# Performance work log

Measured on AMD Instinct MI355X. Metric: run time of the kernel, lower is better.

Reference implementation:

```python
import jax, jax.numpy as jnp
import numpy as np

HEADS = 8

def setup_inputs() -> dict:
    key = jax.random.key(0)
    ks = jax.random.split(key, 10)
    B, C, D, W, H = 4, 256, 12, 12, 12
    dk = C // HEADS
    return {
        "x": jax.random.normal(ks[0], (B, C, D, W, H), jnp.float32),
        "wq": jax.random.normal(ks[1], (C, C), jnp.float32) * 0.05,
        "bq": jax.random.normal(ks[2], (C,), jnp.float32) * 0.05,
        "wk": jax.random.normal(ks[3], (C, C), jnp.float32) * 0.05,
        "bk": jax.random.normal(ks[4], (C,), jnp.float32) * 0.05,
        "wv": jax.random.normal(ks[5], (C, C), jnp.float32) * 0.05,
        "bv": jax.random.normal(ks[6], (C,), jnp.float32) * 0.05,
        "rel_d": jax.random.normal(ks[7], (1, HEADS, dk, D, 1, 1), jnp.float32),
        "rel_h": jax.random.normal(ks[8], (1, HEADS, dk, 1, 1, H), jnp.float32),
        "rel_w": jax.random.normal(ks[9], (1, HEADS, dk, 1, W, 1), jnp.float32),
    }


def reference(x, wq, bq, wk, bk, wv, bv, rel_d, rel_h, rel_w):
    B, C, D, W, H = x.shape
    dk = C // HEADS
    N = D * W * H

    def proj(w, b):
        # Conv3d kernel_size=1 == per-voxel linear over channels
        y = jnp.einsum('bcdwh,oc->bodwh', x, w) + b[None, :, None, None, None]
        return y.reshape(B, HEADS, dk, N)  # [B,h,dk,N]

    q = proj(wq, bq)
    k = proj(wk, bk)
    v = proj(wv, bv)

    # content-content: q^T k -> [B,h,N,N]
    cc = jnp.einsum('bhdn,bhdm->bhnm', q, k)
    # relative-position bias: (rel_h+rel_w+rel_d) broadcasts to [1,h,dk,D,W,H]
    pos = (rel_h + rel_w + rel_d).reshape(1, HEADS, dk, N)
    # content-position: pos^T @ q -> [B,h,N,N]
    cp = jnp.einsum('bhdn,bhdm->bhnm', pos, q)

    attn = jax.nn.softmax(cc + cp, axis=-1)  # [B,h,N,N]
    # out = v @ attn^T -> [B,h,dk,N]
    out = jnp.einsum('bhdn,bhmn->bhdm', v, attn)
    return out.reshape(B, C, D, W, H)
```

## Files before the change

kernel.cpp:

```cpp
#include <hip/hip_runtime.h>
#include <math.h>

#define HEADS 8
#define DK 32
#define B_ 4
#define C_ 256
#define NVOX 1728
#define DE 64
#define PITCH 72
#define XPITCH 136
#define CPITCH 36
#define LOG2E 1.44269504088896f

typedef _Float16 f16x8 __attribute__((ext_vector_type(8)));
typedef float f32x16 __attribute__((ext_vector_type(16)));

__device__ inline float h2f(short s) {
    _Float16 h = *(_Float16*)&s;
    return (float)h;
}
__device__ inline f32x16 mfma32h(f16x8 a, f16x8 b, f32x16 c) {
    return __builtin_amdgcn_mfma_f32_32x32x16_f16(a, b, c, 0, 0, 0);
}

union H8 { _Float16 h[8]; uint4 v; };
union H4 { _Float16 h[4]; uint2 v; };

__global__ void wf16_kernel(const float* __restrict__ wq,
                            const float* __restrict__ wk,
                            const float* __restrict__ wv,
                            short* __restrict__ wf) {
    int idx = blockIdx.x * 256 + threadIdx.x;
    int m = idx >> 16;
    const float* w = (m == 0) ? wq : (m == 1) ? wk : wv;
    _Float16 h = (_Float16)w[idx & 65535];
    wf[idx] = *(short*)&h;
}

__global__ __launch_bounds__(256)
void xf16_kernel(const float* __restrict__ x, short* __restrict__ xf) {
    __shared__ float tile[64][65];
    int nb = blockIdx.x * 64, c0 = blockIdx.y * 64, b = blockIdx.z;
    int t = threadIdx.x;
    const float* xb = x + (size_t)b * C_ * NVOX;
    for (int e = t; e < 4096; e += 256) {
        int ci = e >> 6, nl = e & 63;
        tile[ci][nl] = xb[(size_t)(c0 + ci) * NVOX + nb + nl];
    }
    __syncthreads();
    for (int e = t; e < 512; e += 256) {
        int n = e >> 3, cg = (e & 7) * 8;
        H8 hi;
        #pragma unroll
        for (int j = 0; j < 8; j++) hi.h[j] = (_Float16)tile[cg + j][n];
        size_t off = ((size_t)b * NVOX + nb + n) * C_ + c0 + cg;
        *(uint4*)&xf[off] = hi.v;
    }
}

__global__ void pos_kernel(const float* __restrict__ rel_d,
                           const float* __restrict__ rel_h,
                           const float* __restrict__ rel_w,
                           short* __restrict__ Qf) {
    int t = threadIdx.x;
    int nl = t & 63, dd0 = (t >> 6) * 8;
    int n = blockIdx.x * 64 + nl;
    int h = blockIdx.y, b = blockIdx.z;
    int bh = b * HEADS + h;
    int di = n / 144, wi = (n / 12) % 12, hi = n % 12;
    H8 ph;
    #pragma unroll
    for (int o = 0; o < 8; o++) {
        int hd = h * DK + dd0 + o;
        ph.h[o] = (_Float16)(rel_d[hd * 12 + di] + rel_w[hd * 12 + wi] + rel_h[hd * 12 + hi]);
    }
    *(uint4*)&Qf[((size_t)bh * NVOX + n) * DE + DK + dd0] = ph.v;
}

struct FS {
    union {
        short xs[64 * XPITCH];
        float cbuf[3][64][CPITCH];
    } u;
};

__global__ __launch_bounds__(384, 4)
void fproj_kernel(const short* __restrict__ xf, const short* __restrict__ wf,
                  const float* __restrict__ bq, const float* __restrict__ bk,
                  const float* __restrict__ bv,
                  short* __restrict__ Qf, short* __restrict__ Kf,
                  short* __restrict__ Vf) {
    __shared__ FS sm;
    int nb = blockIdx.x * 64, h = blockIdx.y, b = blockIdx.z;
    int bh = b * HEADS + h;
    int t = threadIdx.x;
    int w = t >> 6, l = t & 63, ln = l & 31, hv = l >> 5;
    int mat = w >> 1, nh = w & 1;

    const short* xb = xf + ((size_t)b * NVOX + nb) * C_;
    const short* wA = wf + ((size_t)mat * C_ + h * DK + ln) * C_;
    int xrow = (nh * 32 + ln) * XPITCH;

    f32x16 acc;
    #pragma unroll
    for (int r = 0; r < 16; r++) acc[r] = 0.f;

    #pragma unroll 1
    for (int ch = 0; ch < 2; ch++) {
        __syncthreads();
        for (int e = t; e < 1024; e += 384) {
            int row = e >> 4, c8 = (e & 15) * 8;
            *(uint4*)&sm.u.xs[row * XPITCH + c8] =
                *(const uint4*)&xb[row * C_ + ch * 128 + c8];
        }
        __syncthreads();
        #pragma unroll 4
        for (int ks = 0; ks < 8; ks++) {
            int kl_ = ks * 16 + hv * 8;
            f16x8 a = *(const f16x8*)&wA[ch * 128 + kl_];
            f16x8 bfr = *(const f16x8*)&sm.u.xs[xrow + kl_];
            acc = mfma32h(a, bfr, acc);
        }
    }
    __syncthreads();

    const float* bias = (mat == 0) ? bq : (mat == 1) ? bk : bv;
    int ncol = nh * 32 + ln;
    #pragma unroll
    for (int q2 = 0; q2 < 4; q2++) {
        float4 cv;
        float* cvp = (float*)&cv;
        #pragma unroll
        for (int m = 0; m < 4; m++) {
            int o_loc = 8 * q2 + 4 * hv + m;
            cvp[m] = acc[4 * q2 + m] + bias[h * DK + o_loc];
        }
        *(float4*)&sm.u.cbuf[mat][ncol][8 * q2 + 4 * hv] = cv;
    }
    __syncthreads();

    if (t < 256) {
        int n = t >> 2, ddg = (t & 3) * 8;
        size_t rowoff = ((size_t)bh * NVOX + nb + n) * DE;
        H8 qh, kh;
        #pragma unroll
        for (int j = 0; j < 8; j++) {
            qh.h[j] = (_Float16)sm.u.cbuf[0][n][ddg + j];
            kh.h[j] = (_Float16)sm.u.cbuf[1][n][ddg + j];
        }
        *(uint4*)&Qf[rowoff + ddg] = qh.v;
        *(uint4*)&Kf[rowoff + ddg] = kh.v;
        *(uint4*)&Kf[rowoff + DK + ddg] = qh.v;
    }
    if (t < 256) {
        int d = t >> 3, ng = (t & 7) * 8;
        H8 vv;
        #pragma unroll
        for (int j = 0; j < 8; j++)
            vv.h[j] = (_Float16)sm.u.cbuf[2][ng + j][d];
        *(uint4*)&Vf[((size_t)bh * DK + d) * NVOX + nb + ng] = vv.v;
    }
}

struct SMem {
    short K[64][PITCH];
    short V[DK][PITCH];
    short P[96][PITCH];
};

__global__ __launch_bounds__(192, 4)
void attn_kernel(const short* __restrict__ Qf, const short* __restrict__ Kf,
                 const short* __restrict__ Vf,
                 short* __restrict__ wsO, float* __restrict__ wsM,
                 float* __restrict__ wsL) {
    __shared__ SMem sm;
    int bx = blockIdx.x;
    int it = bx / 3, jp = bx % 3;
    int h = blockIdx.y, b = blockIdx.z;
    int bh = b * HEADS + h;
    int t = threadIdx.x;
    int w  = t >> 6;
    int l  = t & 63;
    int ln = l & 31;
    int hv = l >> 5;
    int i_loc  = w * 32 + ln;
    int i_glob = it * 96 + i_loc;

    const short* Qp = Qf + (size_t)bh * NVOX * DE;
    const short* Kp = Kf + (size_t)bh * NVOX * DE;
    const short* Vp = Vf + (size_t)bh * DK * NVOX;

    f16x8 qf[4];
    #pragma unroll
    for (int ks = 0; ks < 4; ks++)
        qf[ks] = *(const f16x8*)&Qp[(size_t)i_glob * DE + ks * 16 + hv * 8];

    float mL = -INFINITY;
    float lsum = 0.f;
    f32x16 O;
    #pragma unroll
    for (int r = 0; r < 16; r++) O[r] = 0.f;

    int jt0 = jp * 9, jt1 = jt0 + 9;
    #pragma unroll 1
    for (int jt = jt0; jt < jt1; jt++) {
        int jb = jt * 64;
        __syncthreads();
        for (int e = t; e < 512; e += 192) {
            int row = e >> 3, c = (e & 7) * 8;
            *(uint4*)&sm.K[row][c] = *(const uint4*)&Kp[(size_t)(jb + row) * DE + c];
        }
        for (int e = t; e < 256; e += 192) {
            int d = e >> 3, c = (e & 7) * 8;
            *(uint4*)&sm.V[d][c] = *(const uint4*)&Vp[(size_t)d * NVOX + jb + c];
        }
        __syncthreads();

        f32x16 sc[2];
        #pragma unroll
        for (int js = 0; js < 2; js++) {
            f32x16 s;
            #pragma unroll
            for (int r = 0; r < 16; r++) s[r] = 0.f;
            #pragma unroll
            for (int ks = 0; ks < 4; ks++) {
                f16x8 kfr = *(const f16x8*)&sm.K[js * 32 + ln][ks * 16 + hv * 8];
                s = mfma32h(kfr, qf[ks], s);
            }
            sc[js] = s;
        }

        float mx = sc[0][0];
        #pragma unroll
        for (int js = 0; js < 2; js++)
            #pragma unroll
            for (int r = 0; r < 16; r++) mx = fmaxf(mx, sc[js][r]);
        mx = fmaxf(mx, __shfl_xor(mx, 32));
        float mLn = fmaxf(mL, mx * LOG2E);
        float alpha = exp2f(mL - mLn);
        mL = mLn;
        float ps = 0.f;
        #pragma unroll
        for (int js = 0; js < 2; js++)
            #pragma unroll
            for (int r = 0; r < 16; r++) {
                float p = exp2f(fmaf(sc[js][r], LOG2E, -mLn));
                sc[js][r] = p;
                ps += p;
            }
        ps += __shfl_xor(ps, 32);
        lsum = lsum * alpha + ps;

        #pragma unroll
        for (int js = 0; js < 2; js++)
            #pragma unroll
            for (int g = 0; g < 4; g++) {
                H4 pk;
                #pragma unroll
                for (int m = 0; m < 4; m++) pk.h[m] = (_Float16)sc[js][4 * g + m];
                *(uint2*)&sm.P[i_loc][js * 32 + g * 8 + hv * 4] = pk.v;
            }

        #pragma unroll
        for (int r = 0; r < 16; r++) O[r] *= alpha;
        #pragma unroll
        for (int ks = 0; ks < 4; ks++) {
            f16x8 va = *(const f16x8*)&sm.V[ln][ks * 16 + hv * 8];
            f16x8 pb = *(const f16x8*)&sm.P[i_loc][ks * 16 + hv * 8];
            O = mfma32h(va, pb, O);
        }
    }

    short* Op = wsO + ((size_t)jp * (B_ * HEADS) + bh) * DK * NVOX;
    #pragma unroll
    for (int r = 0; r < 16; r++) {
        int d = (r & 3) + 8 * (r >> 2) + 4 * hv;
        _Float16 oh = (_Float16)O[r];
        Op[(size_t)d * NVOX + i_glob] = *(short*)&oh;
    }
    if (hv == 0) {
        size_t mo = ((size_t)jp * (B_ * HEADS) + bh) * NVOX + i_glob;
        wsM[mo] = mL;
        wsL[mo] = lsum;
    }
}

__global__ void combine_kernel(const short* __restrict__ wsO,
                               const float* __restrict__ wsM,
                               const float* __restrict__ wsL,
                               float* __restrict__ out) {
    int idx = blockIdx.x * 256 + threadIdx.x;
    int i = idx % NVOX;
    int bh = (idx / NVOX) >> 5;
    const size_t oh = (size_t)B_ * HEADS * DK * NVOX;
    const size_t mh = (size_t)B_ * HEADS * NVOX;
    size_t mo = (size_t)bh * NVOX + i;
    float m0 = wsM[mo], m1 = wsM[mh + mo], m2 = wsM[2 * mh + mo];
    float m = fmaxf(fmaxf(m0, m1), m2);
    float a0 = exp2f(m0 - m), a1 = exp2f(m1 - m), a2 = exp2f(m2 - m);
    float num = a0 * h2f(wsO[idx]) + a1 * h2f(wsO[oh + idx]) + a2 * h2f(wsO[2 * oh + idx]);
    float den = a0 * wsL[mo] + a1 * wsL[mh + mo] + a2 * wsL[2 * mh + mo];
    out[idx] = num / den;
}

extern "C" void kernel_launch(void* const* d_in, const int* in_sizes, int n_in,
                              void* d_out, int out_size, void* d_ws, size_t ws_size,
                              hipStream_t stream) {
    const float* x     = (const float*)d_in[0];
    const float* wq    = (const float*)d_in[1];
    const float* bq    = (const float*)d_in[2];
    const float* wk    = (const float*)d_in[3];
    const float* bk    = (const float*)d_in[4];
    const float* wv    = (const float*)d_in[5];
    const float* bv    = (const float*)d_in[6];
    const float* rel_d = (const float*)d_in[7];
    const float* rel_h = (const float*)d_in[8];
    const float* rel_w = (const float*)d_in[9];
    float* out = (float*)d_out;

    size_t qksz = (size_t)B_ * HEADS * NVOX * DE;
    size_t vsz  = (size_t)B_ * HEADS * DK * NVOX;
    short* Qf  = (short*)d_ws;
    short* Kf  = Qf + qksz;
    short* Vf  = Kf + qksz;
    short* wf  = Vf + vsz;
    short* wsO = wf + (size_t)3 * C_ * C_;
    float* wsM = (float*)(wsO + 3 * vsz);
    float* wsL = wsM + 3 * (size_t)B_ * HEADS * NVOX;
    short* xf  = wsO;

    wf16_kernel<<<dim3(3 * C_ * C_ / 256), dim3(256), 0, stream>>>(wq, wk, wv, wf);
    xf16_kernel<<<dim3(NVOX / 64, C_ / 64, B_), dim3(256), 0, stream>>>(x, xf);
    pos_kernel<<<dim3(NVOX / 64, HEADS, B_), dim3(256), 0, stream>>>(
        rel_d, rel_h, rel_w, Qf);
    fproj_kernel<<<dim3(NVOX / 64, HEADS, B_), dim3(384), 0, stream>>>(
        xf, wf, bq, bk, bv, Qf, Kf, Vf);
    attn_kernel<<<dim3(3 * NVOX / 96, HEADS, B_), dim3(192), 0, stream>>>(
        Qf, Kf, Vf, wsO, wsM, wsL);
    combine_kernel<<<dim3((int)(vsz / 256)), dim3(256), 0, stream>>>(wsO, wsM, wsL, out);
}
```

Before: 165.0 us.

## Merge prep kernels, retile attention to 64-row blocks with 2-way KV split

Folds the weight cast, x transpose-cast and positional bias kernels into one prep launch dispatched by block index, removing two launches. Attention blocks shrink from 96 to 64 query rows (2 waves) and the key range is split in two parts of 14 and 13 tiles instead of three parts of 9, so the combine step merges two partials. P packing uses the packed round-toward-zero fp16 convert instead of per-element casts. Together these change grid shape, occupancy and the amount of partial output written and combined.

```diff
diff --git a/kernel.cpp b/kernel.cpp
--- a/kernel.cpp
+++ b/kernel.cpp
@@ -13,6 +13,7 @@
 #define LOG2E 1.44269504088896f
 
 typedef _Float16 f16x8 __attribute__((ext_vector_type(8)));
+typedef __fp16 fp16x2 __attribute__((ext_vector_type(2)));
 typedef float f32x16 __attribute__((ext_vector_type(16)));
 
 __device__ inline float h2f(short s) {
@@ -24,57 +25,61 @@
 }
 
 union H8 { _Float16 h[8]; uint4 v; };
-union H4 { _Float16 h[4]; uint2 v; };
-
-__global__ void wf16_kernel(const float* __restrict__ wq,
-                            const float* __restrict__ wk,
-                            const float* __restrict__ wv,
-                            short* __restrict__ wf) {
-    int idx = blockIdx.x * 256 + threadIdx.x;
-    int m = idx >> 16;
-    const float* w = (m == 0) ? wq : (m == 1) ? wk : wv;
-    _Float16 h = (_Float16)w[idx & 65535];
-    wf[idx] = *(short*)&h;
-}
 
 __global__ __launch_bounds__(256)
-void xf16_kernel(const float* __restrict__ x, short* __restrict__ xf) {
+void prep_kernel(const float* __restrict__ x,
+                 const float* __restrict__ wq, const float* __restrict__ wk,
+                 const float* __restrict__ wv,
+                 const float* __restrict__ rel_d, const float* __restrict__ rel_h,
+                 const float* __restrict__ rel_w,
+                 short* __restrict__ wf, short* __restrict__ xf,
+                 short* __restrict__ Qf) {
     __shared__ float tile[64][65];
-    int nb = blockIdx.x * 64, c0 = blockIdx.y * 64, b = blockIdx.z;
+    int bid = blockIdx.x;
     int t = threadIdx.x;
-    const float* xb = x + (size_t)b * C_ * NVOX;
-    for (int e = t; e < 4096; e += 256) {
-        int ci = e >> 6, nl = e & 63;
-        tile[ci][nl] = xb[(size_t)(c0 + ci) * NVOX + nb + nl];
-    }
-    __syncthreads();
-    for (int e = t; e < 512; e += 256) {
-        int n = e >> 3, cg = (e & 7) * 8;
-        H8 hi;
-        #pragma unroll
-        for (int j = 0; j < 8; j++) hi.h[j] = (_Float16)tile[cg + j][n];
-        size_t off = ((size_t)b * NVOX + nb + n) * C_ + c0 + cg;
-        *(uint4*)&xf[off] = hi.v;
-    }
-}
-
-__global__ void pos_kernel(const float* __restrict__ rel_d,
-                           const float* __restrict__ rel_h,
-                           const float* __restrict__ rel_w,
-                           short* __restrict__ Qf) {
-    int t = threadIdx.x;
-    int nl = t & 63, dd0 = (t >> 6) * 8;
-    int n = blockIdx.x * 64 + nl;
-    int h = blockIdx.y, b = blockIdx.z;
-    int bh = b * HEADS + h;
-    int di = n / 144, wi = (n / 12) % 12, hi = n % 12;
-    H8 ph;
-    #pragma unroll
-    for (int o = 0; o < 8; o++) {
-        int hd = h * DK + dd0 + o;
-        ph.h[o] = (_Float16)(rel_d[hd * 12 + di] + rel_w[hd * 12 + wi] + rel_h[hd * 12 + hi]);
-    }
-    *(uint4*)&Qf[((size_t)bh * NVOX + n) * DE + DK + dd0] = ph.v;
+
+    if (bid < 768) {
+        int idx = bid * 256 + t;
+        int m = idx >> 16;
+        const float* w = (m == 0) ? wq : (m == 1) ? wk : wv;
+        _Float16 h = (_Float16)w[idx & 65535];
+        wf[idx] = *(short*)&h;
+    } else if (bid < 1200) {
+        int q = bid - 768;
+        int nb = (q % 27) * 64;
+        int c0 = ((q / 27) % 4) * 64;
+        int b  = q / 108;
+        const float* xb = x + (size_t)b * C_ * NVOX;
+        for (int e = t; e < 4096; e += 256) {
+            int ci = e >> 6, nl = e & 63;
+            tile[ci][nl] = xb[(size_t)(c0 + ci) * NVOX + nb + nl];
+        }
+        __syncthreads();
+        for (int e = t; e < 512; e += 256) {
+            int n = e >> 3, cg = (e & 7) * 8;
+            H8 hi;
+            #pragma unroll
+            for (int j = 0; j < 8; j++) hi.h[j] = (_Float16)tile[cg + j][n];
+            *(uint4*)&xf[((size_t)b * NVOX + nb + n) * C_ + c0 + cg] = hi.v;
+        }
+    } else {
+        int q = bid - 1200;
+        int nb = (q % 27) * 64;
+        int h  = (q / 27) % 8;
+        int b  = q / 216;
+        int bh = b * HEADS + h;
+        int nl = t & 63, dd0 = (t >> 6) * 8;
+        int n = nb + nl;
+        int di = n / 144, wi = (n / 12) % 12, hi = n % 12;
+        H8 ph;
+        #pragma unroll
+        for (int o = 0; o < 8; o++) {
+            int hd = h * DK + dd0 + o;
+            ph.h[o] = (_Float16)(rel_d[hd * 12 + di] + rel_w[hd * 12 + wi] +
+                                 rel_h[hd * 12 + hi]);
+        }
+        *(uint4*)&Qf[((size_t)bh * NVOX + n) * DE + DK + dd0] = ph.v;
+    }
 }
 
 struct FS {
@@ -165,17 +170,17 @@
 struct SMem {
     short K[64][PITCH];
     short V[DK][PITCH];
-    short P[96][PITCH];
+    short P[64][PITCH];
 };
 
-__global__ __launch_bounds__(192, 4)
+__global__ __launch_bounds__(128, 3)
 void attn_kernel(const short* __restrict__ Qf, const short* __restrict__ Kf,
                  const short* __restrict__ Vf,
                  short* __restrict__ wsO, float* __restrict__ wsM,
                  float* __restrict__ wsL) {
     __shared__ SMem sm;
     int bx = blockIdx.x;
-    int it = bx / 3, jp = bx % 3;
+    int it = bx >> 1, jp = bx & 1;
     int h = blockIdx.y, b = blockIdx.z;
     int bh = b * HEADS + h;
     int t = threadIdx.x;
@@ -184,7 +189,7 @@
     int ln = l & 31;
     int hv = l >> 5;
     int i_loc  = w * 32 + ln;
-    int i_glob = it * 96 + i_loc;
+    int i_glob = it * 64 + i_loc;
 
     const short* Qp = Qf + (size_t)bh * NVOX * DE;
     const short* Kp = Kf + (size_t)bh * NVOX * DE;
@@ -201,16 +206,16 @@
     #pragma unroll
     for (int r = 0; r < 16; r++) O[r] = 0.f;
 
-    int jt0 = jp * 9, jt1 = jt0 + 9;
+    int jt0 = jp ? 14 : 0, jt1 = jp ? 27 : 14;
     #pragma unroll 1
     for (int jt = jt0; jt < jt1; jt++) {
         int jb = jt * 64;
         __syncthreads();
-        for (int e = t; e < 512; e += 192) {
+        for (int e = t; e < 512; e += 128) {
             int row = e >> 3, c = (e & 7) * 8;
             *(uint4*)&sm.K[row][c] = *(const uint4*)&Kp[(size_t)(jb + row) * DE + c];
         }
-        for (int e = t; e < 256; e += 192) {
+        for (int e = t; e < 256; e += 128) {
             int d = e >> 3, c = (e & 7) * 8;
             *(uint4*)&sm.V[d][c] = *(const uint4*)&Vp[(size_t)d * NVOX + jb + c];
         }
@@ -255,9 +260,9 @@
         for (int js = 0; js < 2; js++)
             #pragma unroll
             for (int g = 0; g < 4; g++) {
-                H4 pk;
-                #pragma unroll
-                for (int m = 0; m < 4; m++) pk.h[m] = (_Float16)sc[js][4 * g + m];
+                union { fp16x2 h2[2]; uint2 v; } pk;
+                pk.h2[0] = __builtin_amdgcn_cvt_pkrtz(sc[js][4 * g + 0], sc[js][4 * g + 1]);
+                pk.h2[1] = __builtin_amdgcn_cvt_pkrtz(sc[js][4 * g + 2], sc[js][4 * g + 3]);
                 *(uint2*)&sm.P[i_loc][js * 32 + g * 8 + hv * 4] = pk.v;
             }
 
@@ -295,11 +300,12 @@
     const size_t oh = (size_t)B_ * HEADS * DK * NVOX;
     const size_t mh = (size_t)B_ * HEADS * NVOX;
     size_t mo = (size_t)bh * NVOX + i;
-    float m0 = wsM[mo], m1 = wsM[mh + mo], m2 = wsM[2 * mh + mo];
-    float m = fmaxf(fmaxf(m0, m1), m2);
-    float a0 = exp2f(m0 - m), a1 = exp2f(m1 - m), a2 = exp2f(m2 - m);
-    float num = a0 * h2f(wsO[idx]) + a1 * h2f(wsO[oh + idx]) + a2 * h2f(wsO[2 * oh + idx]);
-    float den = a0 * wsL[mo] + a1 * wsL[mh + mo] + a2 * wsL[2 * mh + mo];
+    float m0 = wsM[mo], m1 = wsM[mh + mo];
+    float l0 = wsL[mo], l1 = wsL[mh + mo];
+    float m = fmaxf(m0, m1);
+    float a0 = exp2f(m0 - m), a1 = exp2f(m1 - m);
+    float num = a0 * h2f(wsO[idx]) + a1 * h2f(wsO[oh + idx]);
+    float den = a0 * l0 + a1 * l1;
     out[idx] = num / den;
 }
 
@@ -325,17 +331,15 @@
     short* Vf  = Kf + qksz;
     short* wf  = Vf + vsz;
     short* wsO = wf + (size_t)3 * C_ * C_;
-    float* wsM = (float*)(wsO + 3 * vsz);
-    float* wsL = wsM + 3 * (size_t)B_ * HEADS * NVOX;
+    float* wsM = (float*)(wsO + 2 * vsz);
+    float* wsL = wsM + 2 * (size_t)B_ * HEADS * NVOX;
     short* xf  = wsO;
 
-    wf16_kernel<<<dim3(3 * C_ * C_ / 256), dim3(256), 0, stream>>>(wq, wk, wv, wf);
-    xf16_kernel<<<dim3(NVOX / 64, C_ / 64, B_), dim3(256), 0, stream>>>(x, xf);
-    pos_kernel<<<dim3(NVOX / 64, HEADS, B_), dim3(256), 0, stream>>>(
-        rel_d, rel_h, rel_w, Qf);
+    prep_kernel<<<dim3(2064), dim3(256), 0, stream>>>(
+        x, wq, wk, wv, rel_d, rel_h, rel_w, wf, xf, Qf);
     fproj_kernel<<<dim3(NVOX / 64, HEADS, B_), dim3(384), 0, stream>>>(
         xf, wf, bq, bk, bv, Qf, Kf, Vf);
-    attn_kernel<<<dim3(3 * NVOX / 96, HEADS, B_), dim3(192), 0, stream>>>(
+    attn_kernel<<<dim3(2 * NVOX / 64, HEADS, B_), dim3(128), 0, stream>>>(
         Qf, Kf, Vf, wsO, wsM, wsL);
     combine_kernel<<<dim3((int)(vsz / 256)), dim3(256), 0, stream>>>(wsO, wsM, wsL, out);
 }
```

Measured after the change: 159.0 us. 1.04x faster.
